# Optimization experiments

Hardware: AMD Instinct MI355X
Metric: run time of the kernel (lower is better)

The kernel has to match this reference:

```python
import jax, jax.numpy as jnp
import numpy as np

B, N, D_IN = 4, 2048, 128
H, HD = 4, 32  # num_heads, head_dim (out_features=128, concat=True)
NEG_SLOPE = 0.2


def setup_inputs() -> dict:
    key = jax.random.key(0)
    kx, kadj, kw, ka = jax.random.split(key, 4)
    x = jax.random.normal(kx, (B, N, D_IN), dtype=jnp.float32)
    adj_mx = jax.random.randint(kadj, (N, N), 0, 2, dtype=jnp.int32)
    # xavier-uniform-ish scaling for params
    W = jax.random.normal(kw, (H * HD, D_IN), dtype=jnp.float32) * (1.0 / np.sqrt(D_IN))
    a = jax.random.normal(ka, (H, 2 * HD, 1), dtype=jnp.float32) * (1.0 / np.sqrt(2 * HD))
    return {"x": x, "adj_mx": adj_mx, "W": W, "a": a}


def reference(x, adj_mx, W, a):
    # x: (B,N,D_in); W: (H*hd, D_in) [nn.Linear weight]; a: (H, 2*hd, 1)
    b, n, _ = x.shape
    hd = a.shape[1] // 2
    h = (x @ W.T).reshape(b, n, H, hd)  # (B,N,H,hd)
    # e_ij = a^T [h_i || h_j] = a1.h_i + a2.h_j  (exact decomposition of the concat-matmul)
    a1 = a[:, :hd, 0]  # (H, hd)
    a2 = a[:, hd:, 0]  # (H, hd)
    ei = jnp.einsum('bnhd,hd->bnh', h, a1)
    ej = jnp.einsum('bnhd,hd->bnh', h, a2)
    e = ei[:, :, None, :] + ej[:, None, :, :]  # (B,N,N,H)
    e = jnp.where(e > 0, e, NEG_SLOPE * e)  # leaky_relu(0.2)
    mask = (adj_mx == 0)[None, :, :, None]  # (1,N,N,1)
    e = jnp.where(mask, -jnp.inf, e)
    attn = jax.nn.softmax(e, axis=2)  # softmax over neighbors j
    # dropout p=0.0 (inference) -> identity
    out = jnp.einsum('bijh,bjhd->bihd', attn, h)  # (B,N,H,hd)
    return out.reshape(b, n, H * hd)  # concat heads
```

## Files before the change

### kernel.cpp

```cpp
#include <hip/hip_runtime.h>
#include <hip/hip_bf16.h>
#include <stdint.h>

#define B 4
#define N 2048
#define DIN 128
#define H 4
#define HD 32
#define NEG 0.2f
#define LOG2E 1.4426950408889634f
#define WINJ 512

typedef __attribute__((ext_vector_type(8))) short short8;
typedef __attribute__((ext_vector_type(4))) float f32x4;

__global__ __launch_bounds__(256) void k_prep(const float* __restrict__ x,
                                              const float* __restrict__ W,
                                              const float* __restrict__ a,
                                              const int* __restrict__ adj,
                                              unsigned short* __restrict__ VT,
                                              float* __restrict__ ei_t,
                                              float* __restrict__ ej_t,
                                              unsigned long long* __restrict__ bits) {
    __shared__ float Wt0[64][64];
    __shared__ float Wt1[64][64];
    __shared__ float xT[64][20];

    const int tid = threadIdx.x;
    if (blockIdx.x >= 512) {
        int t = (blockIdx.x - 512) * 256 + tid;
        int v = adj[t];
        unsigned long long m = __ballot(v != 0);
        if ((tid & 63) == 0) bits[t >> 6] = m;
        return;
    }

    const int lane = tid & 63;
    const int r0 = (tid >> 6) * 4;
    const int c2 = lane;
    const int rowBase = blockIdx.x * 16;
    float acc[4][2];
#pragma unroll
    for (int i = 0; i < 4; ++i) { acc[i][0] = 0.f; acc[i][1] = 0.f; }

    for (int kh = 0; kh < 2; ++kh) {
        __syncthreads();
        {
            const int c = tid & 127;
            const int qb = (tid >> 7) * 8;
            const int ci = c >> 1, pl = c & 1;
            const float4* W4 = (const float4*)W;
#pragma unroll
            for (int q = 0; q < 8; ++q) {
                float4 v = W4[c * 32 + kh * 16 + qb + q];
                int kk = (qb + q) * 4;
                if (pl == 0) {
                    Wt0[kk + 0][ci] = v.x; Wt0[kk + 1][ci] = v.y;
                    Wt0[kk + 2][ci] = v.z; Wt0[kk + 3][ci] = v.w;
                } else {
                    Wt1[kk + 0][ci] = v.x; Wt1[kk + 1][ci] = v.y;
                    Wt1[kk + 2][ci] = v.z; Wt1[kk + 3][ci] = v.w;
                }
            }
        }
        {
            const int rl = tid >> 4;
            const int q = tid & 15;
            float4 v = ((const float4*)x)[(rowBase + rl) * 32 + kh * 16 + q];
            int kk = q * 4;
            xT[kk + 0][rl] = v.x; xT[kk + 1][rl] = v.y;
            xT[kk + 2][rl] = v.z; xT[kk + 3][rl] = v.w;
        }
        __syncthreads();
#pragma unroll 8
        for (int kk = 0; kk < 64; ++kk) {
            float w0 = Wt0[kk][c2];
            float w1 = Wt1[kk][c2];
#pragma unroll
            for (int i = 0; i < 4; ++i) {
                float xv = xT[kk][r0 + i];
                acc[i][0] += xv * w0;
                acc[i][1] += xv * w1;
            }
        }
    }

    const int c0 = 2 * c2;
    const int head = c0 >> 5, d0 = c0 & 31;
    const int b = rowBase >> 11;
    const int n0 = (rowBase & 2047) + r0;
    const int bh = b * 4 + head;

    {
        ushort4 p0, p1;
        unsigned short* q0 = (unsigned short*)&p0;
        unsigned short* q1 = (unsigned short*)&p1;
#pragma unroll
        for (int i = 0; i < 4; ++i) {
            __hip_bfloat16 h0 = __float2bfloat16(acc[i][0]);
            __hip_bfloat16 h1 = __float2bfloat16(acc[i][1]);
            q0[i] = *(unsigned short*)&h0;
            q1[i] = *(unsigned short*)&h1;
        }
        const int wdw = n0 >> 9;
        const int gw  = (n0 >> 3) & 63;
        const int off = n0 & 7;
        const int gs0 = gw ^ (d0 & 7);
        const int gs1 = gw ^ ((d0 + 1) & 7);
        *(ushort4*)&VT[((size_t)bh * 32 + d0) * 2048 + wdw * WINJ + gs0 * 8 + off] = p0;
        *(ushort4*)&VT[((size_t)bh * 32 + d0 + 1) * 2048 + wdw * WINJ + gs1 * 8 + off] = p1;
    }
    {
        float a10 = a[head * 64 + d0],      a11 = a[head * 64 + d0 + 1];
        float a20 = a[head * 64 + 32 + d0], a21 = a[head * 64 + 32 + d0 + 1];
#pragma unroll
        for (int i = 0; i < 4; ++i) {
            float pi = acc[i][0] * a10 + acc[i][1] * a11;
            float pj = acc[i][0] * a20 + acc[i][1] * a21;
#pragma unroll
            for (int off = 1; off < 16; off <<= 1) {
                pi += __shfl_xor(pi, off);
                pj += __shfl_xor(pj, off);
            }
            if ((lane & 15) == 0) {
                ei_t[(size_t)bh * 2048 + n0 + i] = pi * LOG2E;
                ej_t[(size_t)bh * 2048 + n0 + i] = pj * LOG2E;
            }
        }
    }
}

__global__ __launch_bounds__(512) void k_attn_l(const unsigned short* __restrict__ VT,
                                                const float* __restrict__ ei_t,
                                                const float* __restrict__ ej_t,
                                                const unsigned long long* __restrict__ bits,
                                                float* __restrict__ out) {
    __shared__ unsigned short Vs[2][32 * WINJ];
    __shared__ float ejs[2][WINJ];

    const int tid = threadIdx.x;
    const int bid = blockIdx.x;
    const int rt = bid & 15;
    const int head = (bid >> 4) & 3;
    const int b = bid >> 6;
    const int wv = tid >> 6, lane = tid & 63;
    const int lr = lane & 15;
    const int g = lane >> 4;
    const int rowW = rt * 128 + wv * 16;
    const int bh = b * 4 + head;

    const unsigned short* VTb = VT + (size_t)bh * 32 * 2048;
    const float* ejg = ej_t + (size_t)bh * 2048;
    const float eir = ei_t[(size_t)bh * 2048 + rowW + lr];
    const unsigned long long* mrow = bits + (size_t)(rowW + lr) * (N / 64);

    f32x4 acc0 = {0.f, 0.f, 0.f, 0.f};
    f32x4 acc1 = {0.f, 0.f, 0.f, 0.f};
    f32x4 accS = {0.f, 0.f, 0.f, 0.f};
    short8 onesb;
    {
        short ov = (lr == 0) ? (short)0x3F80 : (short)0;
#pragma unroll
        for (int e = 0; e < 8; ++e) onesb[e] = ov;
    }

    {
#pragma unroll
        for (int i = 0; i < 4; ++i) {
            int L = i * 512 + tid, d = L >> 6, gr = L & 63;
            float4 v = *(const float4*)&VTb[(size_t)d * 2048 + gr * 8];
            *(float4*)&Vs[0][(size_t)L * 8] = v;
        }
        if (tid < 128) {
            float4 e = *(const float4*)&ejg[tid * 4];
            *(float4*)&ejs[0][tid * 4] = e;
        }
    }
    __syncthreads();

    for (int w = 0; w < 4; ++w) {
        const int buf = w & 1;
        float4 vr0, vr1, vr2, vr3, er;
        const bool pf = (w < 3);
        if (pf) {
            const unsigned short* src = VTb + (w + 1) * WINJ;
            int L0 = tid,        d0_ = L0 >> 6, g0_ = L0 & 63;
            int L1 = 512 + tid,  d1_ = L1 >> 6, g1_ = L1 & 63;
            int L2 = 1024 + tid, d2_ = L2 >> 6, g2_ = L2 & 63;
            int L3 = 1536 + tid, d3_ = L3 >> 6, g3_ = L3 & 63;
            vr0 = *(const float4*)&src[(size_t)d0_ * 2048 + g0_ * 8];
            vr1 = *(const float4*)&src[(size_t)d1_ * 2048 + g1_ * 8];
            vr2 = *(const float4*)&src[(size_t)d2_ * 2048 + g2_ * 8];
            vr3 = *(const float4*)&src[(size_t)d3_ * 2048 + g3_ * 8];
            if (tid < 128) er = *(const float4*)&ejg[(w + 1) * WINJ + tid * 4];
        }
        __builtin_amdgcn_sched_barrier(0);

        const unsigned short* Vb = &Vs[buf][0];
        const float* ejb = &ejs[buf][0];
#pragma unroll 4
        for (int jl = 0; jl < WINJ; jl += 64) {
            const unsigned long long word = mrow[(w * WINJ + jl) >> 6];
#pragma unroll
            for (int ks = 0; ks < 2; ++ks) {
                const int G = (jl >> 3) + ks * 4 + g;
                const int gs = (G ^ (lr & 7)) * 8;
                short8 b0 = *(const short8*)&Vb[lr * WINJ + gs];
                short8 b1 = *(const short8*)&Vb[(16 + lr) * WINJ + gs];
                const int f = jl + ks * 32 + g * 8;
                float4 ea = *(const float4*)&ejb[f];
                float4 eb = *(const float4*)&ejb[f + 4];
                const unsigned int mb =
                    (unsigned int)(word >> (ks * 32 + g * 8)) & 0xffu;
                float ej8[8] = {ea.x, ea.y, ea.z, ea.w, eb.x, eb.y, eb.z, eb.w};
                short8 pa;
#pragma unroll
                for (int e = 0; e < 8; ++e) {
                    float s = eir + ej8[e];
                    float el = fmaxf(s, NEG * s);
                    float p = ((mb >> e) & 1u) ? __builtin_amdgcn_exp2f(el) : 0.f;
                    __hip_bfloat16 pb = __float2bfloat16(p);
                    pa[e] = (short)*(unsigned short*)&pb;
                }
                acc0 = __builtin_amdgcn_mfma_f32_16x16x32_bf16(pa, b0, acc0, 0, 0, 0);
                acc1 = __builtin_amdgcn_mfma_f32_16x16x32_bf16(pa, b1, acc1, 0, 0, 0);
                accS = __builtin_amdgcn_mfma_f32_16x16x32_bf16(pa, onesb, accS, 0, 0, 0);
            }
        }

        if (pf) {
            const int nbuf = buf ^ 1;
            *(float4*)&Vs[nbuf][(size_t)tid * 8]          = vr0;
            *(float4*)&Vs[nbuf][(size_t)(512 + tid) * 8]  = vr1;
            *(float4*)&Vs[nbuf][(size_t)(1024 + tid) * 8] = vr2;
            *(float4*)&Vs[nbuf][(size_t)(1536 + tid) * 8] = vr3;
            if (tid < 128) *(float4*)&ejs[nbuf][tid * 4] = er;
        }
        __syncthreads();
    }

#pragma unroll
    for (int reg = 0; reg < 4; ++reg) {
        const float sr = __shfl(accS[reg], g * 16);
        const float inv = 1.f / sr;
        const int m = 4 * g + reg;
        float* dst = &out[(size_t)(b * N + rowW + m) * 128 + head * 32 + lr];
        dst[0]  = acc0[reg] * inv;
        dst[16] = acc1[reg] * inv;
    }
}

__global__ __launch_bounds__(256) void k_fused(const float* __restrict__ x,
                                               const int* __restrict__ adj,
                                               const float* __restrict__ W,
                                               const float* __restrict__ a,
                                               float* __restrict__ out) {
    __shared__ float Ws[32][129];
    __shared__ float xs[64][132];
    __shared__ float hs[64][44];
    __shared__ float ejs[64];
    __shared__ float eis[128];
    __shared__ float a1s[32], a2s[32];
    __shared__ unsigned long long mb[128];

    const int tid = threadIdx.x;
    const int bid = blockIdx.x;
    const int rt = bid & 15;
    const int head = (bid >> 4) & 3;
    const int b = bid >> 6;
    const int row0 = rt * 128;

    for (int idx = tid; idx < 32 * 128; idx += 256) {
        int d = idx >> 7, k = idx & 127;
        Ws[d][k] = W[(head * 32 + d) * 128 + k];
    }
    if (tid < 32) a1s[tid] = a[head * 64 + tid];
    else if (tid < 64) a2s[tid - 32] = a[head * 64 + tid];
    __syncthreads();

    for (int c0 = 0; c0 < 128; c0 += 64) {
        __syncthreads();
        {
            int jj = tid >> 2, k0 = (tid & 3) * 32;
            const float4* src = (const float4*)&x[(b * N + row0 + c0 + jj) * 128 + k0];
#pragma unroll
            for (int q = 0; q < 8; ++q) *(float4*)&xs[jj][k0 + q * 4] = src[q];
        }
        __syncthreads();
        {
            int jj = tid >> 2, db = (tid & 3) * 8;
#pragma unroll
            for (int dd = 0; dd < 8; ++dd) {
                float s = 0.f;
                for (int k = 0; k < 128; ++k) s += xs[jj][k] * Ws[db + dd][k];
                hs[jj][db + dd] = s;
            }
        }
        __syncthreads();
        if (tid < 64) {
            float s = 0.f;
#pragma unroll
            for (int d = 0; d < 32; ++d) s += hs[tid][d] * a1s[d];
            eis[c0 + tid] = s;
        }
    }

    const int dgrp = tid & 3, d0 = dgrp * 8;
    const int rseg = tid >> 2;
    float acc[2][8];
    float sacc[2] = {0.f, 0.f};
#pragma unroll
    for (int k = 0; k < 2; ++k)
#pragma unroll
        for (int d = 0; d < 8; ++d) acc[k][d] = 0.f;

    for (int jc = 0; jc < N; jc += 64) {
        __syncthreads();
        {
            int jj = tid >> 2, k0 = (tid & 3) * 32;
            const float4* src = (const float4*)&x[(b * N + jc + jj) * 128 + k0];
#pragma unroll
            for (int q = 0; q < 8; ++q) *(float4*)&xs[jj][k0 + q * 4] = src[q];
        }
        {
            int wv = tid >> 6, lane = tid & 63;
            for (int p = 0; p < 32; ++p) {
                int il = p * 4 + wv;
                unsigned long long m = __ballot(adj[(row0 + il) * N + jc + lane] != 0);
                if (lane == 0) mb[il] = m;
            }
        }
        __syncthreads();
        {
            int jj = tid >> 2, db = (tid & 3) * 8;
#pragma unroll
            for (int dd = 0; dd < 8; ++dd) {
                float s = 0.f;
                for (int k = 0; k < 128; ++k) s += xs[jj][k] * Ws[db + dd][k];
                hs[jj][db + dd] = s;
            }
        }
        __syncthreads();
        if (tid < 64) {
            float s = 0.f;
#pragma unroll
            for (int d = 0; d < 32; ++d) s += hs[tid][d] * a2s[d];
            ejs[tid] = s;
        }
        __syncthreads();
        for (int jj = 0; jj < 64; ++jj) {
            float ejv = ejs[jj];
            float hv[8];
#pragma unroll
            for (int d = 0; d < 8; ++d) hv[d] = hs[jj][d0 + d];
#pragma unroll
            for (int k = 0; k < 2; ++k) {
                int il = rseg * 2 + k;
                float s = eis[il] + ejv;
                float el = s > 0.f ? s : NEG * s;
                float p = ((mb[il] >> jj) & 1ull) ? __expf(el) : 0.f;
                sacc[k] += p;
#pragma unroll
                for (int d = 0; d < 8; ++d) acc[k][d] += p * hv[d];
            }
        }
    }
#pragma unroll
    for (int k = 0; k < 2; ++k) {
        int il = rseg * 2 + k;
        float inv = 1.f / sacc[k];
        float* dst = &out[(b * N + row0 + il) * 128 + head * 32 + d0];
#pragma unroll
        for (int d = 0; d < 8; ++d) dst[d] = acc[k][d] * inv;
    }
}

extern "C" void kernel_launch(void* const* d_in, const int* in_sizes, int n_in,
                              void* d_out, int out_size, void* d_ws, size_t ws_size,
                              hipStream_t stream) {
    const float* x = nullptr; const int* adj = nullptr;
    const float* W = nullptr; const float* a = nullptr;
    for (int i = 0; i < n_in; ++i) {
        switch (in_sizes[i]) {
            case B * N * DIN:  x   = (const float*)d_in[i]; break;
            case N * N:        adj = (const int*)d_in[i];   break;
            case H * HD * DIN: W   = (const float*)d_in[i]; break;
            case H * 2 * HD:   a   = (const float*)d_in[i]; break;
        }
    }
    float* out = (float*)d_out;

    const size_t szVT = (size_t)B * H * HD * N * 2;
    const size_t szE  = (size_t)B * H * N * 4;
    const size_t szBits = (size_t)N * (N / 64) * 8;
    const size_t need = szVT + 2 * szE + szBits;

    if (ws_size >= need) {
        char* ws = (char*)d_ws;
        unsigned short* VT = (unsigned short*)ws;
        float* ei_t = (float*)(ws + szVT);
        float* ej_t = (float*)(ws + szVT + szE);
        unsigned long long* bits = (unsigned long long*)(ws + szVT + 2 * szE);

        k_prep<<<512 + (N * N) / 256, 256, 0, stream>>>(x, W, a, adj, VT, ei_t, ej_t, bits);
        k_attn_l<<<256, 512, 0, stream>>>(VT, ei_t, ej_t, bits, out);
    } else {
        k_fused<<<256, 256, 0, stream>>>(x, adj, W, a, out);
    }
}
```

Measured before the change: 111.7 us.

## Split attention into smaller blocks, transpose mask bits, and raise MFMA priority

The attention kernel now runs 512 blocks of 256 threads over 64 rows each, with 256-column windows in place of 256 blocks of 512 threads over 512-column windows. The packed adjacency bitmask is stored transposed so each window's mask words are read in one coalesced load per lane and passed around with shuffles. MFMA sections are wrapped in s_setprio, and the inner loop is fully unrolled. The aim is better CU occupancy and latency hiding, and fewer scattered mask loads. The cost is more window iterations and barriers, plus K/V tiles loaded by twice as many blocks.

```diff
diff --git a/kernel.cpp b/kernel.cpp
--- a/kernel.cpp
+++ b/kernel.cpp
@@ -9,10 +9,11 @@
 #define HD 32
 #define NEG 0.2f
 #define LOG2E 1.4426950408889634f
-#define WINJ 512
+#define WINJ 256
 
 typedef __attribute__((ext_vector_type(8))) short short8;
 typedef __attribute__((ext_vector_type(4))) float f32x4;
+
 
 __global__ __launch_bounds__(256) void k_prep(const float* __restrict__ x,
                                               const float* __restrict__ W,
@@ -21,7 +22,7 @@
                                               unsigned short* __restrict__ VT,
                                               float* __restrict__ ei_t,
                                               float* __restrict__ ej_t,
-                                              unsigned long long* __restrict__ bits) {
+                                              unsigned long long* __restrict__ bitsT) {
     __shared__ float Wt0[64][64];
     __shared__ float Wt1[64][64];
     __shared__ float xT[64][20];
@@ -31,7 +32,10 @@
         int t = (blockIdx.x - 512) * 256 + tid;
         int v = adj[t];
         unsigned long long m = __ballot(v != 0);
-        if ((tid & 63) == 0) bits[t >> 6] = m;
+        if ((tid & 63) == 0) {
+            int row = t >> 11, jw = (t >> 6) & 31;
+            bitsT[(size_t)jw * 2048 + row] = m;
+        }
         return;
     }
 
@@ -86,10 +90,10 @@
     }
 
     const int c0 = 2 * c2;
-    const int head = c0 >> 5, d0 = c0 & 31;
+    const int headT = c0 >> 5, d0 = c0 & 31;
     const int b = rowBase >> 11;
     const int n0 = (rowBase & 2047) + r0;
-    const int bh = b * 4 + head;
+    const int bh = b * 4 + headT;
 
     {
         ushort4 p0, p1;
@@ -102,8 +106,8 @@
             q0[i] = *(unsigned short*)&h0;
             q1[i] = *(unsigned short*)&h1;
         }
-        const int wdw = n0 >> 9;
-        const int gw  = (n0 >> 3) & 63;
+        const int wdw = n0 >> 8;
+        const int gw  = (n0 >> 3) & 31;
         const int off = n0 & 7;
         const int gs0 = gw ^ (d0 & 7);
         const int gs1 = gw ^ ((d0 + 1) & 7);
@@ -111,8 +115,8 @@
         *(ushort4*)&VT[((size_t)bh * 32 + d0 + 1) * 2048 + wdw * WINJ + gs1 * 8 + off] = p1;
     }
     {
-        float a10 = a[head * 64 + d0],      a11 = a[head * 64 + d0 + 1];
-        float a20 = a[head * 64 + 32 + d0], a21 = a[head * 64 + 32 + d0 + 1];
+        float a10 = a[headT * 64 + d0],      a11 = a[headT * 64 + d0 + 1];
+        float a20 = a[headT * 64 + 32 + d0], a21 = a[headT * 64 + 32 + d0 + 1];
 #pragma unroll
         for (int i = 0; i < 4; ++i) {
             float pi = acc[i][0] * a10 + acc[i][1] * a11;
@@ -130,29 +134,28 @@
     }
 }
 
-__global__ __launch_bounds__(512) void k_attn_l(const unsigned short* __restrict__ VT,
+__global__ __launch_bounds__(256) void k_attn_w(const unsigned short* __restrict__ VT,
                                                 const float* __restrict__ ei_t,
                                                 const float* __restrict__ ej_t,
-                                                const unsigned long long* __restrict__ bits,
+                                                const unsigned long long* __restrict__ bitsT,
                                                 float* __restrict__ out) {
-    __shared__ unsigned short Vs[2][32 * WINJ];
-    __shared__ float ejs[2][WINJ];
+    __shared__ __align__(16) unsigned short Vs[2][32 * WINJ];
+    __shared__ __align__(16) float ejs[2][WINJ];
 
     const int tid = threadIdx.x;
     const int bid = blockIdx.x;
-    const int rt = bid & 15;
-    const int head = (bid >> 4) & 3;
-    const int b = bid >> 6;
+    const int rt = bid & 31;
+    const int head = (bid >> 5) & 3;
+    const int b = bid >> 7;
     const int wv = tid >> 6, lane = tid & 63;
     const int lr = lane & 15;
     const int g = lane >> 4;
-    const int rowW = rt * 128 + wv * 16;
+    const int rowW = rt * 64 + wv * 16;
     const int bh = b * 4 + head;
 
     const unsigned short* VTb = VT + (size_t)bh * 32 * 2048;
     const float* ejg = ej_t + (size_t)bh * 2048;
     const float eir = ei_t[(size_t)bh * 2048 + rowW + lr];
-    const unsigned long long* mrow = bits + (size_t)(rowW + lr) * (N / 64);
 
     f32x4 acc0 = {0.f, 0.f, 0.f, 0.f};
     f32x4 acc1 = {0.f, 0.f, 0.f, 0.f};
@@ -167,46 +170,45 @@
     {
 #pragma unroll
         for (int i = 0; i < 4; ++i) {
-            int L = i * 512 + tid, d = L >> 6, gr = L & 63;
+            int L = i * 256 + tid, d = L >> 5, gr = L & 31;
             float4 v = *(const float4*)&VTb[(size_t)d * 2048 + gr * 8];
             *(float4*)&Vs[0][(size_t)L * 8] = v;
         }
-        if (tid < 128) {
+        if (tid < 64) {
             float4 e = *(const float4*)&ejg[tid * 4];
             *(float4*)&ejs[0][tid * 4] = e;
         }
     }
     __syncthreads();
 
-    for (int w = 0; w < 4; ++w) {
+    for (int w = 0; w < 8; ++w) {
         const int buf = w & 1;
+        const unsigned long long wreg =
+            bitsT[(size_t)(w * 4 + g) * 2048 + rowW + lr];
+
         float4 vr0, vr1, vr2, vr3, er;
-        const bool pf = (w < 3);
+        const bool pf = (w < 7);
         if (pf) {
             const unsigned short* src = VTb + (w + 1) * WINJ;
-            int L0 = tid,        d0_ = L0 >> 6, g0_ = L0 & 63;
-            int L1 = 512 + tid,  d1_ = L1 >> 6, g1_ = L1 & 63;
-            int L2 = 1024 + tid, d2_ = L2 >> 6, g2_ = L2 & 63;
-            int L3 = 1536 + tid, d3_ = L3 >> 6, g3_ = L3 & 63;
-            vr0 = *(const float4*)&src[(size_t)d0_ * 2048 + g0_ * 8];
-            vr1 = *(const float4*)&src[(size_t)d1_ * 2048 + g1_ * 8];
-            vr2 = *(const float4*)&src[(size_t)d2_ * 2048 + g2_ * 8];
-            vr3 = *(const float4*)&src[(size_t)d3_ * 2048 + g3_ * 8];
-            if (tid < 128) er = *(const float4*)&ejg[(w + 1) * WINJ + tid * 4];
+            vr0 = *(const float4*)&src[(size_t)((tid)        >> 5) * 2048 + ((tid)        & 31) * 8];
+            vr1 = *(const float4*)&src[(size_t)((256 + tid)  >> 5) * 2048 + ((256 + tid)  & 31) * 8];
+            vr2 = *(const float4*)&src[(size_t)((512 + tid)  >> 5) * 2048 + ((512 + tid)  & 31) * 8];
+            vr3 = *(const float4*)&src[(size_t)((768 + tid)  >> 5) * 2048 + ((768 + tid)  & 31) * 8];
+            if (tid < 64) er = *(const float4*)&ejg[(w + 1) * WINJ + tid * 4];
         }
         __builtin_amdgcn_sched_barrier(0);
 
         const unsigned short* Vb = &Vs[buf][0];
         const float* ejb = &ejs[buf][0];
-#pragma unroll 4
+#pragma unroll
         for (int jl = 0; jl < WINJ; jl += 64) {
-            const unsigned long long word = mrow[(w * WINJ + jl) >> 6];
+            const unsigned long long word = __shfl(wreg, (jl >> 6) * 16 + lr);
 #pragma unroll
             for (int ks = 0; ks < 2; ++ks) {
-                const int G = (jl >> 3) + ks * 4 + g;
-                const int gs = (G ^ (lr & 7)) * 8;
-                short8 b0 = *(const short8*)&Vb[lr * WINJ + gs];
-                short8 b1 = *(const short8*)&Vb[(16 + lr) * WINJ + gs];
+                const int gw_ = (jl >> 3) + ks * 4 + g;
+                const int slot = gw_ ^ (lr & 7);
+                short8 b0 = *(const short8*)&Vb[lr * WINJ + slot * 8];
+                short8 b1 = *(const short8*)&Vb[(16 + lr) * WINJ + slot * 8];
                 const int f = jl + ks * 32 + g * 8;
                 float4 ea = *(const float4*)&ejb[f];
                 float4 eb = *(const float4*)&ejb[f + 4];
@@ -222,19 +224,21 @@
                     __hip_bfloat16 pb = __float2bfloat16(p);
                     pa[e] = (short)*(unsigned short*)&pb;
                 }
+                __builtin_amdgcn_s_setprio(1);
                 acc0 = __builtin_amdgcn_mfma_f32_16x16x32_bf16(pa, b0, acc0, 0, 0, 0);
                 acc1 = __builtin_amdgcn_mfma_f32_16x16x32_bf16(pa, b1, acc1, 0, 0, 0);
                 accS = __builtin_amdgcn_mfma_f32_16x16x32_bf16(pa, onesb, accS, 0, 0, 0);
+                __builtin_amdgcn_s_setprio(0);
             }
         }
 
         if (pf) {
             const int nbuf = buf ^ 1;
             *(float4*)&Vs[nbuf][(size_t)tid * 8]          = vr0;
-            *(float4*)&Vs[nbuf][(size_t)(512 + tid) * 8]  = vr1;
-            *(float4*)&Vs[nbuf][(size_t)(1024 + tid) * 8] = vr2;
-            *(float4*)&Vs[nbuf][(size_t)(1536 + tid) * 8] = vr3;
-            if (tid < 128) *(float4*)&ejs[nbuf][tid * 4] = er;
+            *(float4*)&Vs[nbuf][(size_t)(256 + tid) * 8]  = vr1;
+            *(float4*)&Vs[nbuf][(size_t)(512 + tid) * 8]  = vr2;
+            *(float4*)&Vs[nbuf][(size_t)(768 + tid) * 8]  = vr3;
+            if (tid < 64) *(float4*)&ejs[nbuf][tid * 4] = er;
         }
         __syncthreads();
     }
@@ -400,10 +404,10 @@
         unsigned short* VT = (unsigned short*)ws;
         float* ei_t = (float*)(ws + szVT);
         float* ej_t = (float*)(ws + szVT + szE);
-        unsigned long long* bits = (unsigned long long*)(ws + szVT + 2 * szE);
-
-        k_prep<<<512 + (N * N) / 256, 256, 0, stream>>>(x, W, a, adj, VT, ei_t, ej_t, bits);
-        k_attn_l<<<256, 512, 0, stream>>>(VT, ei_t, ej_t, bits, out);
+        unsigned long long* bitsT = (unsigned long long*)(ws + szVT + 2 * szE);
+
+        k_prep<<<512 + (N * N) / 256, 256, 0, stream>>>(x, W, a, adj, VT, ei_t, ej_t, bitsT);
+        k_attn_w<<<512, 256, 0, stream>>>(VT, ei_t, ej_t, bitsT, out);
     } else {
         k_fused<<<256, 256, 0, stream>>>(x, adj, W, a, out);
     }
```

After: 111.0 us. No clear change (-0.6%).
